# Optimization experiments

Hardware: AMD Instinct MI355X
Metric: run time of the kernel (lower is better)

## Reference

```python
import jax, jax.numpy as jnp
import numpy as np

B, T, D_MODEL = 2, 2048, 1024
H, D = 16, 64
NEG = -1e9


def setup_inputs() -> dict:
    key = jax.random.key(0)
    k1, k2, k3 = jax.random.split(key, 3)
    x = jax.random.normal(k1, (B, T, D_MODEL), dtype=jnp.float32)
    # causal additive bias: 0 at valid (j<=i), large negative otherwise
    causal = jnp.tril(jnp.ones((T, T), dtype=bool))
    mask = jnp.where(causal, 0.0, NEG).astype(jnp.float32)[None, None]
    # params (torch Linear no-bias; stored as [in, out] so y = x @ W)
    W_qkv = jax.random.normal(k2, (D_MODEL, H * 5 * D), dtype=jnp.float32) / np.sqrt(D_MODEL)
    W_out = jax.random.normal(k3, (H * D, D_MODEL), dtype=jnp.float32) / np.sqrt(H * D)
    lam = jnp.full((H,), 0.8, dtype=jnp.float32)
    return {"x": x, "mask": mask, "W_qkv": W_qkv, "W_out": W_out, "lam": lam}


def reference(x, mask, W_qkv, W_out, lam):
    scale = np.sqrt(D).astype(np.float32)
    qkv = (x @ W_qkv).reshape(B, T, H, 5 * D)          # (B,T,H,5D)
    q1, q2, k1, k2, v = (qkv[..., i * D:(i + 1) * D] for i in range(5))
    # scores: (B,H,T,T)
    s1 = jnp.einsum('bihd,bjhd->bhij', q1, k1) / scale + mask
    s2 = jnp.einsum('bihd,bjhd->bhij', q2, k2) / scale + mask
    a1 = jax.nn.softmax(s1, axis=-1)
    a2 = jax.nn.softmax(s2, axis=-1)
    lam_c = jnp.clip(lam, 0.0, 1.0)[None, :, None, None]
    attn = a1 - lam_c * a2
    out = jnp.einsum('bhij,bjhd->bihd', attn, v).reshape(B, T, H * D)
    return out @ W_out
```

## Files before the change

kernel.cpp:

```cpp
#include <hip/hip_runtime.h>


typedef __attribute__((ext_vector_type(8))) short short8;
typedef __attribute__((ext_vector_type(4))) float floatx4;
typedef __attribute__((ext_vector_type(2))) unsigned uintx2;

#define MFMA16(A_, B_, C_) __builtin_amdgcn_mfma_f32_16x16x32_bf16((A_), (B_), (C_), 0, 0, 0)

__device__ __forceinline__ unsigned short f2bf(float f) {
  unsigned u;
  __builtin_memcpy(&u, &f, 4);
  u += 0x7fffu + ((u >> 16) & 1u);
  return (unsigned short)(u >> 16);
}

__device__ __forceinline__ unsigned packbf2(float a, float b) {
  unsigned ua, ub;
  __builtin_memcpy(&ua, &a, 4);
  __builtin_memcpy(&ub, &b, 4);
  ua += 0x8000u;
  ub += 0x8000u;
  return __builtin_amdgcn_perm(ub, ua, 0x07060302u);
}

__device__ __forceinline__ void gload16(const unsigned short* g, void* l) {
  __builtin_amdgcn_global_load_lds(
      (const __attribute__((address_space(1))) void*)g,
      (__attribute__((address_space(3))) void*)l, 16, 0, 0);
}

__global__ __launch_bounds__(256) void cast_f32_bf16(const float* __restrict__ in,
                                                     unsigned short* __restrict__ out) {
  size_t i = ((size_t)blockIdx.x * 256 + threadIdx.x) * 8;
  float4 a0 = *(const float4*)(in + i);
  float4 a1 = *(const float4*)(in + i + 4);
  short8 v = {(short)f2bf(a0.x), (short)f2bf(a0.y), (short)f2bf(a0.z), (short)f2bf(a0.w),
              (short)f2bf(a1.x), (short)f2bf(a1.y), (short)f2bf(a1.z), (short)f2bf(a1.w)};
  *(short8*)(out + i) = v;
}

__global__ __launch_bounds__(256) void transpose_both(const float* __restrict__ wqkv,
                                                      unsigned short* __restrict__ wqkvT,
                                                      const float* __restrict__ wout,
                                                      unsigned short* __restrict__ woutT) {
  __shared__ unsigned short t[32][33];
  int bid = blockIdx.x;
  const float* in;
  unsigned short* out;
  int R = 1024, C;
  int bx, by;
  if (bid < 5120) {
    in = wqkv; out = wqkvT; C = 5120;
    bx = bid % 160; by = bid / 160;
  } else {
    bid -= 5120;
    in = wout; out = woutT; C = 1024;
    bx = bid % 32; by = bid / 32;
  }
  int c0 = bx * 32, r0 = by * 32;
  int tx = threadIdx.x & 31, ty = threadIdx.x >> 5;
#pragma unroll
  for (int i = 0; i < 4; i++) {
    int r = ty + i * 8;
    t[r][tx] = f2bf(in[(size_t)(r0 + r) * C + c0 + tx]);
  }
  __syncthreads();
#pragma unroll
  for (int i = 0; i < 4; i++) {
    int r = ty + i * 8;
    out[(size_t)(c0 + r) * R + r0 + tx] = t[tx][r];
  }
}

__global__ __launch_bounds__(512, 2) void gemm_qkv(const unsigned short* __restrict__ A,
                                                   const unsigned short* __restrict__ Bt,
                                                   unsigned short* __restrict__ qkbuf,
                                                   unsigned short* __restrict__ vtbuf) {
  const int tid = threadIdx.x;
  const int wave = tid >> 6, lane = tid & 63, lane15 = lane & 15, quad = lane >> 4;
  const int wm = wave >> 2, wn = wave & 3;
  const int bn = blockIdx.x % 20, bm = blockIdx.x / 20;
  const int row0 = bm * 256, col0 = bn * 256;
  __shared__ __align__(16) short SMEM[65536];
  floatx4 acc[8][4] = {};

  const int srow = lane >> 3;
  const int sseg = ((lane & 7) ^ srow) * 8;
  const unsigned short* gA = A + (size_t)(row0 + srow) * 1024 + sseg;
  const unsigned short* gB = Bt + (size_t)(col0 + srow) * 1024 + sseg;

  auto stage = [&](int bufidx, int kt) {
#pragma unroll
    for (int u = 0; u < 4; u++) {
      const int c = wave * 4 + u;
      gload16(gA + (size_t)c * 8192 + kt, &SMEM[bufidx * 16384 + c * 512]);
      gload16(gB + (size_t)c * 8192 + kt, &SMEM[32768 + bufidx * 16384 + c * 512]);
    }
  };

  stage(0, 0);
  stage(1, 64);

  const int swz = (lane15 & 7) << 3;
  for (int t = 0; t < 16; t++) {
    if (t < 15) {
      asm volatile("s_waitcnt vmcnt(8)" ::: "memory");
    } else {
      asm volatile("s_waitcnt vmcnt(0)" ::: "memory");
    }
    __builtin_amdgcn_s_barrier();
    const short* Ab = &SMEM[(t & 1) * 16384];
    const short* Bb = &SMEM[32768 + (t & 1) * 16384];
#pragma unroll
    for (int kh = 0; kh < 2; kh++) {
      short8 bf[4];
#pragma unroll
      for (int nt = 0; nt < 4; nt++)
        bf[nt] =
            *(const short8*)&Bb[(wn * 64 + nt * 16 + lane15) * 64 + ((kh * 32 + quad * 8) ^ swz)];
#pragma unroll
      for (int mh = 0; mh < 2; mh++) {
        short8 af[4];
#pragma unroll
        for (int mt = 0; mt < 4; mt++)
          af[mt] = *(const short8*)&Ab[(wm * 128 + mh * 64 + mt * 16 + lane15) * 64 +
                                       ((kh * 32 + quad * 8) ^ swz)];
        __builtin_amdgcn_s_setprio(1);
#pragma unroll
        for (int mt = 0; mt < 4; mt++)
#pragma unroll
          for (int nt = 0; nt < 4; nt++)
            acc[mh * 4 + mt][nt] = MFMA16(af[mt], bf[nt], acc[mh * 4 + mt][nt]);
        __builtin_amdgcn_s_setprio(0);
      }
    }
    __builtin_amdgcn_s_barrier();
    if (t + 2 < 16) stage(t & 1, (t + 2) * 64);
  }

  const int G = bn * 4 + wn;
  const int g5 = G % 5, h = G / 5;
  short* Svt = SMEM;
  if (g5 != 4) {
#pragma unroll
    for (int m = 0; m < 8; m++)
#pragma unroll
      for (int nt = 0; nt < 4; nt++)
#pragma unroll
        for (int r = 0; r < 4; r++) {
          const int row = row0 + wm * 128 + m * 16 + quad * 4 + r;
          const int cq = g5 * 64 + nt * 16 + lane15;
          qkbuf[(size_t)row * 4096 + h * 256 + cq] = f2bf(acc[m][nt][r]);
        }
  } else {
#pragma unroll
    for (int m = 0; m < 8; m++)
#pragma unroll
      for (int nt = 0; nt < 4; nt++)
#pragma unroll
        for (int r = 0; r < 4; r++)
          Svt[(nt * 16 + lane15) * 264 + wm * 128 + m * 16 + quad * 4 + r] =
              (short)f2bf(acc[m][nt][r]);
  }
  __syncthreads();
  if ((bn % 5) != 0) {
    const int wnV = (4 + bn) % 5;
    const int hV = (4 * bn + wnV) / 5;
    const int bb = row0 >> 11, t0 = row0 & 2047;
    const int d = tid >> 3, sg = (tid & 7) * 32;
    unsigned short* gdst = vtbuf + (size_t)((bb * 16 + hV) * 64 + d) * 2048 + t0 + sg;
#pragma unroll
    for (int u2 = 0; u2 < 4; u2++)
      *(short8*)(gdst + u2 * 8) = *(const short8*)&Svt[d * 264 + sg + u2 * 8];
  }
}

__global__ __launch_bounds__(256, 2) void attn_kernel(const unsigned short* __restrict__ qk,
                                                      const unsigned short* __restrict__ vt,
                                                      const float* __restrict__ lam,
                                                      unsigned short* __restrict__ attnout) {
  const int tid = threadIdx.x;
  const int wave = tid >> 6, lane = tid & 63, lane15 = lane & 15, quad = lane >> 4;
  const int bid = blockIdx.x;
  const int pr = bid >> 5, bh = bid & 31;
  const int h = bh & 15, b = bh >> 4;

  __shared__ __align__(16) short K12s[2][64 * 128];
  __shared__ __align__(16) short Vts[2][64 * 64];
  __shared__ __align__(16) short Ps[4][16 * 72];

  const float lamv = fminf(fmaxf(lam[h], 0.0f), 1.0f);

  const unsigned short* kbase = qk + (size_t)(b * 2048) * 4096 + h * 256 + 128;
  const unsigned short* vbase = vt + (size_t)((b * 16 + h) * 64) * 2048;

  const int klr = lane >> 4, kcp = (lane & 15) * 16;
  const int vlr = lane >> 3, vcp = (lane & 7) * 16;
  const int swz = (lane15 & 7) << 4;

  for (int sg = 0; sg < 2; sg++) {
    const int qt = sg ? (31 - pr) : pr;
    const int njt = qt + 1;
    const int qsub = qt * 4 + wave;

    const int qrow0 = qt * 64 + wave * 16;
    const unsigned short* qb = qk + (size_t)(b * 2048 + qrow0 + lane15) * 4096 + h * 256;
    const short8 q1f0 = *(const short8*)(qb + quad * 8);
    const short8 q1f1 = *(const short8*)(qb + 32 + quad * 8);
    const short8 q2f0 = *(const short8*)(qb + 64 + quad * 8);
    const short8 q2f1 = *(const short8*)(qb + 96 + quad * 8);

    floatx4 o1[4] = {}, o2[4] = {};
    float lp1 = 0.f, lp2 = 0.f;

    if (sg) __syncthreads();

#pragma unroll
    for (int u = 0; u < 4; u++) {
      const int c = u * 4 + wave, row = 4 * c + klr;
      gload16(kbase + (size_t)row * 4096 + ((kcp ^ ((row & 7) << 4)) >> 1), &K12s[0][c * 512]);
    }
#pragma unroll
    for (int u = 0; u < 2; u++) {
      const int c = u * 4 + wave, row = 8 * c + vlr;
      gload16(vbase + (size_t)row * 2048 + ((vcp ^ ((row & 7) << 4)) >> 1), &Vts[0][c * 512]);
    }

    int cur = 0;
    for (int jt = 0; jt < njt; jt++) {
      __syncthreads();
      if (jt + 1 < njt) {
        const int nb = cur ^ 1;
#pragma unroll
        for (int u = 0; u < 4; u++) {
          const int c = u * 4 + wave, row = 4 * c + klr;
          gload16(kbase + (size_t)((jt + 1) * 64 + row) * 4096 + ((kcp ^ ((row & 7) << 4)) >> 1),
                  &K12s[nb][c * 512]);
        }
#pragma unroll
        for (int u = 0; u < 2; u++) {
          const int c = u * 4 + wave, row = 8 * c + vlr;
          gload16(vbase + (size_t)row * 2048 + (jt + 1) * 64 + ((vcp ^ ((row & 7) << 4)) >> 1),
                  &Vts[nb][c * 512]);
        }
      }

      const int rel = qsub - 4 * jt;

      short8 vf[4][2];
#pragma unroll
      for (int nt = 0; nt < 4; nt++) {
        const short* vr = &Vts[cur][(nt * 16 + lane15) * 64];
        vf[nt][0] = *(const short8*)(vr + (((quad * 16) ^ swz) >> 1));
        vf[nt][1] = *(const short8*)(vr + (((64 + quad * 16) ^ swz) >> 1));
      }

      short* P = &Ps[wave][0];

#pragma unroll
      for (int mat = 0; mat < 2; mat++) {
        const int koffB = mat ? 128 : 0;
        const short8 qf0 = mat ? q2f0 : q1f0;
        const short8 qf1 = mat ? q2f1 : q1f1;
        float* lp = mat ? &lp2 : &lp1;
        floatx4* oo = mat ? o2 : o1;

#pragma unroll
        for (int ms = 0; ms < 4; ms++) {
          unsigned w0 = 0, w1 = 0;
          if (ms <= rel) {
            const short* kr = &K12s[cur][(ms * 16 + lane15) * 128];
            short8 k0 = *(const short8*)(kr + (((koffB + quad * 16) ^ swz) >> 1));
            short8 k1 = *(const short8*)(kr + (((koffB + 64 + quad * 16) ^ swz) >> 1));
            floatx4 s = {0.f, 0.f, 0.f, 0.f};
            s = MFMA16(k0, qf0, s);
            s = MFMA16(k1, qf1, s);
            float e[4];
#pragma unroll
            for (int r = 0; r < 4; r++)
              e[r] = __builtin_amdgcn_exp2f(s[r] * 0.18033688011112042f);
            if (ms == rel) {
              const int jq = quad * 4;
#pragma unroll
              for (int r = 0; r < 4; r++) e[r] = (jq + r <= lane15) ? e[r] : 0.0f;
            }
            *lp += (e[0] + e[1]) + (e[2] + e[3]);
            w0 = packbf2(e[0], e[1]);
            w1 = packbf2(e[2], e[3]);
          }
          uintx2 wv = {w0, w1};
          *(uintx2*)&P[lane15 * 72 + ms * 16 + quad * 4] = wv;
        }
        const short8 pa0 = *(const short8*)&P[lane15 * 72 + quad * 8];
        const short8 pa1 = *(const short8*)&P[lane15 * 72 + 32 + quad * 8];
#pragma unroll
        for (int nt = 0; nt < 4; nt++) oo[nt] = MFMA16(pa0, vf[nt][0], oo[nt]);
        if (rel >= 2) {
#pragma unroll
          for (int nt = 0; nt < 4; nt++) oo[nt] = MFMA16(pa1, vf[nt][1], oo[nt]);
        }
      }
      cur ^= 1;
    }

    lp1 += __shfl_xor(lp1, 16, 64);
    lp1 += __shfl_xor(lp1, 32, 64);
    lp2 += __shfl_xor(lp2, 16, 64);
    lp2 += __shfl_xor(lp2, 32, 64);

#pragma unroll
    for (int r = 0; r < 4; r++) {
      const float l1 = __shfl(lp1, quad * 4 + r, 64);
      const float l2 = __shfl(lp2, quad * 4 + r, 64);
      const float rl1 = __builtin_amdgcn_rcpf(l1);
      const float rl2 = lamv * __builtin_amdgcn_rcpf(l2);
      const int row = b * 2048 + qrow0 + quad * 4 + r;
#pragma unroll
      for (int nt = 0; nt < 4; nt++) {
        float v = o1[nt][r] * rl1 - o2[nt][r] * rl2;
        attnout[(size_t)row * 1024 + h * 64 + nt * 16 + lane15] = f2bf(v);
      }
    }
  }
}

__global__ __launch_bounds__(256) void gemm_out(const unsigned short* __restrict__ A,
                                                const unsigned short* __restrict__ Bt,
                                                float* __restrict__ Cout) {
  const int tid = threadIdx.x;
  const int wave = tid >> 6, lane = tid & 63, lane15 = lane & 15, quad = lane >> 4;
  const int wr = wave >> 1, wc = wave & 1;
  const int bn = blockIdx.x & 7, bm = blockIdx.x >> 3;
  const int row0 = bm * 64, col0 = bn * 128;
  __shared__ __align__(16) short As[64 * 64];
  __shared__ __align__(16) short Bs[128 * 64];
  floatx4 acc[2][4] = {};
  const int slr = lane >> 3, scl = (lane & 7) * 8;
  for (int kt = 0; kt < 1024; kt += 64) {
    __syncthreads();
#pragma unroll
    for (int u = 0; u < 2; u++) {
      const int c = wave * 2 + u;
      gload16(A + (size_t)(row0 + 8 * c + slr) * 1024 + kt + scl, &As[c * 512]);
    }
#pragma unroll
    for (int u = 0; u < 4; u++) {
      const int c = wave * 4 + u;
      gload16(Bt + (size_t)(col0 + 8 * c + slr) * 1024 + kt + scl, &Bs[c * 512]);
    }
    __syncthreads();
#pragma unroll
    for (int kh = 0; kh < 2; kh++) {
      short8 af[2], bf[4];
#pragma unroll
      for (int mt = 0; mt < 2; mt++)
        af[mt] = *(const short8*)&As[(wr * 32 + mt * 16 + lane15) * 64 + kh * 32 + quad * 8];
#pragma unroll
      for (int nt = 0; nt < 4; nt++)
        bf[nt] = *(const short8*)&Bs[(wc * 64 + nt * 16 + lane15) * 64 + kh * 32 + quad * 8];
#pragma unroll
      for (int mt = 0; mt < 2; mt++)
#pragma unroll
        for (int nt = 0; nt < 4; nt++) acc[mt][nt] = MFMA16(af[mt], bf[nt], acc[mt][nt]);
    }
  }
#pragma unroll
  for (int mt = 0; mt < 2; mt++)
#pragma unroll
    for (int nt = 0; nt < 4; nt++)
#pragma unroll
      for (int r = 0; r < 4; r++) {
        int row = row0 + wr * 32 + mt * 16 + quad * 4 + r;
        int col = col0 + wc * 64 + nt * 16 + lane15;
        Cout[(size_t)row * 1024 + col] = acc[mt][nt][r];
      }
}

extern "C" void kernel_launch(void* const* d_in, const int* in_sizes, int n_in,
                              void* d_out, int out_size, void* d_ws, size_t ws_size,
                              hipStream_t stream) {
  const float* x = (const float*)d_in[0];
  const float* Wqkv = (const float*)d_in[2];
  const float* Wout = (const float*)d_in[3];
  const float* lam = (const float*)d_in[4];
  float* out = (float*)d_out;

  unsigned short* ws = (unsigned short*)d_ws;
  unsigned short* WqkvT = ws;
  unsigned short* WoutT = WqkvT + (size_t)5120 * 1024;
  unsigned short* qkbuf = WoutT + (size_t)1024 * 1024;
  unsigned short* vtbuf = qkbuf + (size_t)4096 * 4096;
  unsigned short* xb = vtbuf + (size_t)2 * 16 * 64 * 2048;
  unsigned short* attnbuf = xb;

  cast_f32_bf16<<<2048, 256, 0, stream>>>(x, xb);
  transpose_both<<<5120 + 1024, 256, 0, stream>>>(Wqkv, WqkvT, Wout, WoutT);
  gemm_qkv<<<16 * 20, 512, 0, stream>>>(xb, WqkvT, qkbuf, vtbuf);
  attn_kernel<<<512, 256, 0, stream>>>(qkbuf, vtbuf, lam, attnbuf);
  gemm_out<<<64 * 8, 256, 0, stream>>>(attnbuf, WoutT, out);
}
```

Before: 251.6 us.

## Process paired causal query tiles concurrently in one 8-wave block sharing K/V tiles

The attention kernel used to handle its two causal query tiles (pr and 31-pr) one after the other in a 4-wave block, reloading K/V for each. It now launches 512-thread blocks in which waves 0-3 take one query tile and waves 4-7 the other, streaming K/V once for the longer tile. Waves whose tile is already finished skip compute but still join the barriers. This is meant to cut K/V global and LDS traffic and add more waves for latency hiding. In exchange, the raised launch bounds may squeeze registers, idle waves still pay barrier costs, and 66 KB of LDS per block limits residency.

New measurement: 244.7 us. 1.03x faster.

```diff
diff --git a/kernel.cpp b/kernel.cpp
--- a/kernel.cpp
+++ b/kernel.cpp
@@ -175,19 +175,22 @@
   }
 }
 
-__global__ __launch_bounds__(256, 2) void attn_kernel(const unsigned short* __restrict__ qk,
+__global__ __launch_bounds__(512, 4) void attn_kernel(const unsigned short* __restrict__ qk,
                                                       const unsigned short* __restrict__ vt,
                                                       const float* __restrict__ lam,
                                                       unsigned short* __restrict__ attnout) {
   const int tid = threadIdx.x;
   const int wave = tid >> 6, lane = tid & 63, lane15 = lane & 15, quad = lane >> 4;
+  const int w4 = wave & 3, wt = wave >> 2;
   const int bid = blockIdx.x;
-  const int pr = bid >> 5, bh = bid & 31;
+  const int u = bid >> 8, c = bid & 255, k = c >> 5, bh = c & 31;
+  const int pr = u ? (15 - k) : k;
   const int h = bh & 15, b = bh >> 4;
+  const int qt = wt ? (31 - pr) : pr;
 
   __shared__ __align__(16) short K12s[2][64 * 128];
   __shared__ __align__(16) short Vts[2][64 * 64];
-  __shared__ __align__(16) short Ps[4][16 * 72];
+  __shared__ __align__(16) short Ps[8][16 * 72];
 
   const float lamv = fminf(fmaxf(lam[h], 0.0f), 1.0f);
 
@@ -198,55 +201,49 @@
   const int vlr = lane >> 3, vcp = (lane & 7) * 16;
   const int swz = (lane15 & 7) << 4;
 
-  for (int sg = 0; sg < 2; sg++) {
-    const int qt = sg ? (31 - pr) : pr;
-    const int njt = qt + 1;
-    const int qsub = qt * 4 + wave;
-
-    const int qrow0 = qt * 64 + wave * 16;
-    const unsigned short* qb = qk + (size_t)(b * 2048 + qrow0 + lane15) * 4096 + h * 256;
-    const short8 q1f0 = *(const short8*)(qb + quad * 8);
-    const short8 q1f1 = *(const short8*)(qb + 32 + quad * 8);
-    const short8 q2f0 = *(const short8*)(qb + 64 + quad * 8);
-    const short8 q2f1 = *(const short8*)(qb + 96 + quad * 8);
-
-    floatx4 o1[4] = {}, o2[4] = {};
-    float lp1 = 0.f, lp2 = 0.f;
-
-    if (sg) __syncthreads();
-
-#pragma unroll
-    for (int u = 0; u < 4; u++) {
-      const int c = u * 4 + wave, row = 4 * c + klr;
-      gload16(kbase + (size_t)row * 4096 + ((kcp ^ ((row & 7) << 4)) >> 1), &K12s[0][c * 512]);
-    }
-#pragma unroll
-    for (int u = 0; u < 2; u++) {
-      const int c = u * 4 + wave, row = 8 * c + vlr;
-      gload16(vbase + (size_t)row * 2048 + ((vcp ^ ((row & 7) << 4)) >> 1), &Vts[0][c * 512]);
-    }
-
-    int cur = 0;
-    for (int jt = 0; jt < njt; jt++) {
-      __syncthreads();
-      if (jt + 1 < njt) {
-        const int nb = cur ^ 1;
-#pragma unroll
-        for (int u = 0; u < 4; u++) {
-          const int c = u * 4 + wave, row = 4 * c + klr;
-          gload16(kbase + (size_t)((jt + 1) * 64 + row) * 4096 + ((kcp ^ ((row & 7) << 4)) >> 1),
-                  &K12s[nb][c * 512]);
-        }
-#pragma unroll
-        for (int u = 0; u < 2; u++) {
-          const int c = u * 4 + wave, row = 8 * c + vlr;
-          gload16(vbase + (size_t)row * 2048 + (jt + 1) * 64 + ((vcp ^ ((row & 7) << 4)) >> 1),
-                  &Vts[nb][c * 512]);
-        }
-      }
-
-      const int rel = qsub - 4 * jt;
-
+  const int qrow0 = qt * 64 + w4 * 16;
+  const unsigned short* qb = qk + (size_t)(b * 2048 + qrow0 + lane15) * 4096 + h * 256;
+  const short8 q1f0 = *(const short8*)(qb + quad * 8);
+  const short8 q1f1 = *(const short8*)(qb + 32 + quad * 8);
+  const short8 q2f0 = *(const short8*)(qb + 64 + quad * 8);
+  const short8 q2f1 = *(const short8*)(qb + 96 + quad * 8);
+
+  floatx4 o1[4] = {}, o2[4] = {};
+  float lp1 = 0.f, lp2 = 0.f;
+
+  const int qsub = qt * 4 + w4;
+  const int njt = 32 - pr;
+
+#pragma unroll
+  for (int u2 = 0; u2 < 2; u2++) {
+    const int ck = wave * 2 + u2, row = 4 * ck + klr;
+    gload16(kbase + (size_t)row * 4096 + ((kcp ^ ((row & 7) << 4)) >> 1), &K12s[0][ck * 512]);
+  }
+  {
+    const int cv = wave, row = 8 * cv + vlr;
+    gload16(vbase + (size_t)row * 2048 + ((vcp ^ ((row & 7) << 4)) >> 1), &Vts[0][cv * 512]);
+  }
+
+  int cur = 0;
+  for (int jt = 0; jt < njt; jt++) {
+    __syncthreads();
+    if (jt + 1 < njt) {
+      const int nb = cur ^ 1;
+#pragma unroll
+      for (int u2 = 0; u2 < 2; u2++) {
+        const int ck = wave * 2 + u2, row = 4 * ck + klr;
+        gload16(kbase + (size_t)((jt + 1) * 64 + row) * 4096 + ((kcp ^ ((row & 7) << 4)) >> 1),
+                &K12s[nb][ck * 512]);
+      }
+      {
+        const int cv = wave, row = 8 * cv + vlr;
+        gload16(vbase + (size_t)row * 2048 + (jt + 1) * 64 + ((vcp ^ ((row & 7) << 4)) >> 1),
+                &Vts[nb][cv * 512]);
+      }
+    }
+
+    const int rel = qsub - 4 * jt;
+    if (rel >= 0) {
       short8 vf[4][2];
 #pragma unroll
       for (int nt = 0; nt < 4; nt++) {
@@ -300,26 +297,26 @@
           for (int nt = 0; nt < 4; nt++) oo[nt] = MFMA16(pa1, vf[nt][1], oo[nt]);
         }
       }
-      cur ^= 1;
-    }
-
-    lp1 += __shfl_xor(lp1, 16, 64);
-    lp1 += __shfl_xor(lp1, 32, 64);
-    lp2 += __shfl_xor(lp2, 16, 64);
-    lp2 += __shfl_xor(lp2, 32, 64);
-
-#pragma unroll
-    for (int r = 0; r < 4; r++) {
-      const float l1 = __shfl(lp1, quad * 4 + r, 64);
-      const float l2 = __shfl(lp2, quad * 4 + r, 64);
-      const float rl1 = __builtin_amdgcn_rcpf(l1);
-      const float rl2 = lamv * __builtin_amdgcn_rcpf(l2);
-      const int row = b * 2048 + qrow0 + quad * 4 + r;
-#pragma unroll
-      for (int nt = 0; nt < 4; nt++) {
-        float v = o1[nt][r] * rl1 - o2[nt][r] * rl2;
-        attnout[(size_t)row * 1024 + h * 64 + nt * 16 + lane15] = f2bf(v);
-      }
+    }
+    cur ^= 1;
+  }
+
+  lp1 += __shfl_xor(lp1, 16, 64);
+  lp1 += __shfl_xor(lp1, 32, 64);
+  lp2 += __shfl_xor(lp2, 16, 64);
+  lp2 += __shfl_xor(lp2, 32, 64);
+
+#pragma unroll
+  for (int r = 0; r < 4; r++) {
+    const float l1 = __shfl(lp1, quad * 4 + r, 64);
+    const float l2 = __shfl(lp2, quad * 4 + r, 64);
+    const float rl1 = __builtin_amdgcn_rcpf(l1);
+    const float rl2 = lamv * __builtin_amdgcn_rcpf(l2);
+    const int row = b * 2048 + qrow0 + quad * 4 + r;
+#pragma unroll
+    for (int nt = 0; nt < 4; nt++) {
+      float v = o1[nt][r] * rl1 - o2[nt][r] * rl2;
+      attnout[(size_t)row * 1024 + h * 64 + nt * 16 + lane15] = f2bf(v);
     }
   }
 }
@@ -396,6 +393,6 @@
   cast_f32_bf16<<<2048, 256, 0, stream>>>(x, xb);
   transpose_both<<<5120 + 1024, 256, 0, stream>>>(Wqkv, WqkvT, Wout, WoutT);
   gemm_qkv<<<16 * 20, 512, 0, stream>>>(xb, WqkvT, qkbuf, vtbuf);
-  attn_kernel<<<512, 256, 0, stream>>>(qkbuf, vtbuf, lam, attnbuf);
+  attn_kernel<<<512, 512, 0, stream>>>(qkbuf, vtbuf, lam, attnbuf);
   gemm_out<<<64 * 8, 256, 0, stream>>>(attnbuf, WoutT, out);
 }
```
